# Performance work log

Measured on AMD Instinct MI355X. Metric: run time of the kernel, lower is better.

The kernel has to match this reference:

```python
import jax, jax.numpy as jnp
import numpy as np

H, W = 256, 256          # resolution from __init__ default
FLOW_SCALING = 256.0     # max(resolution)
MAX_TS = 1.0             # events timestamps normalized to [0, 1]
EPS = 1e-9


def _warp_event(events, flow, tref, ts_weights=None):
    """Bilinear splatting of motion-compensated events into per-polarity IWE.
    events: [B,N,4] (ts,x,y,p); flow: [B,N,2]. Returns [B,2,H,W]."""
    ts = events[..., 0]                      # [B,N]
    x = events[..., 1]
    y = events[..., 2]
    pol = events[..., 3]
    # warped (floating-point) positions
    wx = x + (tref - ts) * flow[..., 0] * FLOW_SCALING
    wy = y + (tref - ts) * flow[..., 1] * FLOW_SCALING
    lx = jnp.floor(wx)
    ty = jnp.floor(wy)
    # 4 bilinear corners: [B,4,N]
    cx = jnp.stack([lx, lx + 1.0, lx, lx + 1.0], axis=1)
    cy = jnp.stack([ty, ty, ty + 1.0, ty + 1.0], axis=1)
    w = (jnp.maximum(0.0, 1.0 - jnp.abs(wx[:, None, :] - cx))
         * jnp.maximum(0.0, 1.0 - jnp.abs(wy[:, None, :] - cy)))
    inb = (cx >= 0) & (cx <= W - 1) & (cy >= 0) & (cy <= H - 1)
    w = jnp.where(inb, w, 0.0)
    if ts_weights is not None:               # optional per-event weight (ts)
        w = w * ts_weights[:, None, :]
    flat = (jnp.clip(cy, 0, H - 1) * W + jnp.clip(cx, 0, W - 1)).astype(jnp.int32)

    def splat(f, ww):  # scatter-add one batch element into flat H*W histogram
        return jnp.zeros(H * W, dtype=w.dtype).at[f.reshape(-1)].add(ww.reshape(-1))

    pos_w = jnp.where((pol == 1)[:, None, :], w, 0.0)
    neg_w = jnp.where((pol == -1)[:, None, :], w, 0.0)
    iwe_pos = jax.vmap(splat)(flat, pos_w).reshape(-1, H, W)
    iwe_neg = jax.vmap(splat)(flat, neg_w).reshape(-1, H, W)
    return jnp.stack([iwe_pos, iwe_neg], axis=1)  # [B,2,H,W]


def _warp_contrast(tref, flow, events):
    iwe = _warp_event(events, flow, tref)
    ts_iwe = _warp_event(events, flow, tref, ts_weights=events[..., 0])
    ts_iwe = ts_iwe / (iwe + EPS)
    loss = (ts_iwe ** 2).sum(axis=(1, 2, 3))           # [B]
    non_zero = ((iwe[:, 0] + iwe[:, 1]) > 0).astype(iwe.dtype)
    return loss / non_zero.sum(axis=(1, 2))


def setup_inputs() -> dict:
    key = jax.random.key(0)
    k1, k2, k3, k4, k5 = jax.random.split(key, 5)
    B, N = 2, 1_000_000
    ts = jax.random.uniform(k1, (B, N))
    x = jax.random.uniform(k2, (B, N)) * (W - 1)
    y = jax.random.uniform(k3, (B, N)) * (H - 1)
    p = jnp.where(jax.random.bernoulli(k4, 0.5, (B, N)), 1.0, -1.0)
    events = jnp.stack([ts, x, y, p], axis=-1).astype(jnp.float32)  # [B,N,4]
    flow = (jax.random.normal(k5, (B, N, 2)) * 0.05).astype(jnp.float32)
    return {"events": events, "flow": flow}


def reference(events, flow):
    # temporal contrast-maximization loss: forward + backward warp per pass
    fw = _warp_contrast(MAX_TS, flow, events).sum() / MAX_TS ** 2
    bw = _warp_contrast(0.0, flow, events).sum() / MAX_TS ** 2
    return fw + bw
```

## Files before the change

### kernel.cpp

```cpp
#include <hip/hip_runtime.h>

#define HH 256
#define WW 256
#define HW (HH * WW)
#define BATCH 2
#define NPASS 2
#define EPSF 1e-9f
#define FLOW_SCALE 256.0f

#define NBLK1 1024
#define NCH 2
#define SCAP 1280
#define CAP 2144
#define FPSCALE 16777216.0f
#define FPINV (1.0f / 16777216.0f)


__global__ __launch_bounds__(256) void ew_bin12(
    const float4* __restrict__ events, const float2* __restrict__ flow,
    float* __restrict__ recs, unsigned* __restrict__ tbl, int N) {
  const int b = blockIdx.y;
  const int gblk = b * NBLK1 + blockIdx.x;
  events += (size_t)b * N;
  flow += (size_t)b * N;
  const int EB = (N + NBLK1 - 1) / NBLK1;
  const int i0 = blockIdx.x * EB;
  const int iend = (i0 + EB < N) ? i0 + EB : N;
  const int CEB = (EB + NCH - 1) / NCH;

  __shared__ float stage[SCAP * 3];
  __shared__ unsigned cnt[128], scan[128], start[128], cur[128];
  __shared__ unsigned s_base;
  if (threadIdx.x == 0) s_base = 0u;

  float* __restrict__ myrecs = recs + (size_t)gblk * CAP * 3;

  for (int c = 0; c < NCH; ++c) {
    const int j0 = i0 + c * CEB;
    int j1 = j0 + CEB;
    if (j1 > iend) j1 = iend;
    if (threadIdx.x < 128) {
      cnt[threadIdx.x] = 0u;
      cur[threadIdx.x] = 0u;
    }
    __syncthreads();

    float rwx[2][2], rwy[2][2], rtsp[2];
    unsigned renc[2][2];
    renc[0][0] = renc[0][1] = renc[1][0] = renc[1][1] = 0u;
#pragma unroll
    for (int s = 0; s < 2; ++s) {
      const int i = j0 + s * 256 + (int)threadIdx.x;
      if (i < j1) {
        const float4 e = events[i];
        const float2 f = flow[i];
        rtsp[s] = copysignf(e.x, e.w);
#pragma unroll
        for (int pass = 0; pass < 2; ++pass) {
          const float tref = (pass == 0) ? 1.0f : 0.0f;
          const float dt = tref - e.x;
          const float wx = fmaf(dt * f.x, FLOW_SCALE, e.y);
          const float wy = fmaf(dt * f.y, FLOW_SCALE, e.z);
          rwx[s][pass] = wx;
          rwy[s][pass] = wy;
          const int lx = (int)floorf(wx), ly = (int)floorf(wy);
          int tx = 0, nx = 0, ty = 0, ny = 0;
          if ((unsigned)lx < 256u) {
            tx = lx >> 5;
            nx = ((unsigned)(lx + 1) < 256u && (((lx + 1) >> 5) != tx)) ? 2 : 1;
          } else if ((unsigned)(lx + 1) < 256u) {
            tx = 0;
            nx = 1;
          }
          if ((unsigned)ly < 256u) {
            ty = ly >> 5;
            ny = ((unsigned)(ly + 1) < 256u && (((ly + 1) >> 5) != ty)) ? 2 : 1;
          } else if ((unsigned)(ly + 1) < 256u) {
            ty = 0;
            ny = 1;
          }
          renc[s][pass] = (unsigned)tx | ((unsigned)ty << 3) |
                          ((unsigned)nx << 6) | ((unsigned)ny << 8);
          for (int a = 0; a < ny; ++a)
            for (int c2 = 0; c2 < nx; ++c2)
              atomicAdd(&cnt[pass * 64 + (ty + a) * 8 + tx + c2], 1u);
        }
      }
    }
    __syncthreads();

    if (threadIdx.x < 64) {
      const int l = threadIdx.x;
      unsigned a = cnt[l], bq = cnt[64 + l];
      for (int off = 1; off < 64; off <<= 1) {
        const unsigned ta = __shfl_up(a, off, 64);
        const unsigned tb = __shfl_up(bq, off, 64);
        if (l >= off) {
          a += ta;
          bq += tb;
        }
      }
      const unsigned tot0 = __shfl(a, 63, 64);
      scan[l] = a;
      scan[64 + l] = bq + tot0;
    }
    __syncthreads();

    const unsigned base = s_base;
    unsigned total = scan[127];
    if (total > SCAP) total = SCAP;
    if (total > CAP - base) total = CAP - base;
    if (threadIdx.x < 128) {
      const unsigned c0 = cnt[threadIdx.x];
      const unsigned st = scan[threadIdx.x] - c0;
      unsigned ec = 0u;
      if (st < total) ec = (c0 < total - st) ? c0 : (total - st);
      start[threadIdx.x] = st;
      tbl[((size_t)gblk * 128 + threadIdx.x) * NCH + c] =
          (base + st) | (ec << 16);
    }
    __syncthreads();

#pragma unroll
    for (int s = 0; s < 2; ++s) {
      const int i = j0 + s * 256 + (int)threadIdx.x;
      if (i < j1) {
        const float tsp = rtsp[s];
#pragma unroll
        for (int pass = 0; pass < 2; ++pass) {
          const unsigned enc = renc[s][pass];
          const int nx = (enc >> 6) & 3;
          const int ny = (enc >> 8) & 3;
          if (nx == 0 || ny == 0) continue;
          const int tx = enc & 7;
          const int ty = (enc >> 3) & 7;
          const float wx = rwx[s][pass];
          const float wy = rwy[s][pass];
          for (int a = 0; a < ny; ++a)
            for (int c2 = 0; c2 < nx; ++c2) {
              const int bin = pass * 64 + (ty + a) * 8 + tx + c2;
              const unsigned pos = start[bin] + atomicAdd(&cur[bin], 1u);
              if (pos < total) {
                stage[pos * 3 + 0] = wx;
                stage[pos * 3 + 1] = wy;
                stage[pos * 3 + 2] = tsp;
              }
            }
        }
      }
    }
    __syncthreads();

    const unsigned nf = total * 3;
    float* __restrict__ dst = myrecs + (size_t)base * 3;
    for (unsigned j = threadIdx.x; j < nf; j += 256) dst[j] = stage[j];
    __syncthreads();
    if (threadIdx.x == 0) s_base = base + total;
  }
}

__global__ __launch_bounds__(512) void ew_accum10(
    const float* __restrict__ recs, const uint2* __restrict__ tbl2,
    unsigned long long* __restrict__ histU, int nrep) {
  const int gbin = blockIdx.x;
  const int rep = blockIdx.y;
  const int b = gbin >> 7;
  const int bin127 = gbin & 127;
  const int pass = (gbin >> 6) & 1;
  const int tile = gbin & 63;
  const int tx0 = (tile & 7) * 32;
  const int ty0 = (tile >> 3) * 32;
  const int pb = pass * 2 + b;

  __shared__ unsigned long long lds64[2048];
  for (int j = threadIdx.x; j < 2048; j += 512) lds64[j] = 0ull;
  __syncthreads();

  const int bpr = NBLK1 / nrep;
  const int blk0 = rep * bpr;
  const int grp = threadIdx.x >> 3;
  const int lane = threadIdx.x & 7;
  for (int r = blk0 + grp; r < blk0 + bpr; r += 64) {
    const int gblk = b * NBLK1 + r;
    const float* __restrict__ blkrec = recs + (size_t)gblk * CAP * 3;
    const uint2 tv = tbl2[(size_t)gblk * 128 + bin127];
    const unsigned tvs[2] = {tv.x, tv.y};
#pragma unroll
    for (int c = 0; c < NCH; ++c) {
      const unsigned st = tvs[c] & 0xffffu;
      const unsigned ct = tvs[c] >> 16;
      for (unsigned k = lane; k < ct; k += 8) {
        const float wx = blkrec[(st + k) * 3 + 0];
        const float wy = blkrec[(st + k) * 3 + 1];
        const unsigned tb = __float_as_uint(blkrec[(st + k) * 3 + 2]);
        const int spol = (int)(tb >> 31);
        const float ts = __uint_as_float(tb & 0x7fffffffu);
        const int lx = (int)floorf(wx), ly = (int)floorf(wy);
        const float fx = wx - (float)lx;
        const float fy = wy - (float)ly;
        const float wxs[2] = {1.0f - fx, fx};
        const float wys[2] = {1.0f - fy, fy};
#pragma unroll
        for (int dy = 0; dy < 2; ++dy) {
          const int lcy = ly + dy - ty0;
          if ((unsigned)lcy >= 32u) continue;
#pragma unroll
          for (int dx = 0; dx < 2; ++dx) {
            const int lcx = lx + dx - tx0;
            if ((unsigned)lcx >= 32u) continue;
            const float w = wxs[dx] * wys[dy];
            const unsigned wq = __float2uint_rn(w * FPSCALE);
            const unsigned tq = __float2uint_rn(w * ts * FPSCALE);
            const unsigned long long v =
                ((unsigned long long)wq << 32) | (unsigned long long)tq;
            atomicAdd(&lds64[spol * 1024 + lcy * 32 + lcx], v);
          }
        }
      }
    }
  }
  __syncthreads();

  for (int j = threadIdx.x; j < 2048; j += 512) {
    const int spol = j >> 10;
    const int within = j & 1023;
    const size_t px = (size_t)(ty0 + (within >> 5)) * WW + tx0 + (within & 31);
    histU[(((size_t)rep * 4 + pb) * 2 + spol) * HW + px] = lds64[j];
  }
}

__global__ __launch_bounds__(256) void ew_reduce7(
    const unsigned long long* __restrict__ histU, float* __restrict__ partial,
    int nrep) {
  const int sub = blockIdx.x;
  const int pb = blockIdx.y;
  float loss = 0.0f, nz = 0.0f;
  for (int k = threadIdx.x; k < 1024; k += 256) {
    const int pix = sub * 1024 + k;
    unsigned long long v0 = 0ull, v1 = 0ull;
    for (int r = 0; r < nrep; ++r) {
      v0 += histU[(((size_t)r * 4 + pb) * 2 + 0) * HW + pix];
      v1 += histU[(((size_t)r * 4 + pb) * 2 + 1) * HW + pix];
    }
    const float ip = (float)(unsigned)(v0 >> 32) * FPINV;
    const float tp = (float)(unsigned)(v0 & 0xffffffffull) * FPINV;
    const float in_ = (float)(unsigned)(v1 >> 32) * FPINV;
    const float tn = (float)(unsigned)(v1 & 0xffffffffull) * FPINV;
    const float a = tp / (ip + EPSF);
    const float d = tn / (in_ + EPSF);
    loss += a * a + d * d;
    nz += ((ip + in_) > 0.0f) ? 1.0f : 0.0f;
  }
  for (int off = 32; off > 0; off >>= 1) {
    loss += __shfl_down(loss, off, 64);
    nz += __shfl_down(nz, off, 64);
  }
  __shared__ float sl[4], sn[4];
  const int wid = threadIdx.x >> 6;
  if ((threadIdx.x & 63) == 0) {
    sl[wid] = loss;
    sn[wid] = nz;
  }
  __syncthreads();
  if (threadIdx.x == 0) {
    partial[pb * 64 + sub] = sl[0] + sl[1] + sl[2] + sl[3];
    partial[256 + pb * 64 + sub] = sn[0] + sn[1] + sn[2] + sn[3];
  }
}

__global__ void ew_final3(const float* __restrict__ partial,
                          float* __restrict__ out) {
  if (threadIdx.x == 0 && blockIdx.x == 0) {
    float s = 0.0f;
    for (int pb = 0; pb < 4; ++pb) {
      float L = 0.0f, Z = 0.0f;
      for (int j = 0; j < 64; ++j) {
        L += partial[pb * 64 + j];
        Z += partial[256 + pb * 64 + j];
      }
      s += L / Z;
    }
    out[0] = s;
  }
}

#define HIST_FLOATS (NPASS * BATCH * 4 * HW)

__global__ __launch_bounds__(256) void ew_scatter(
    const float4* __restrict__ events, const float2* __restrict__ flow,
    float* __restrict__ hist, int N) {
  const int b = blockIdx.y;
  events += (size_t)b * N;
  flow += (size_t)b * N;
  float* __restrict__ hb = hist + (size_t)b * 4 * HW;
  for (int i = blockIdx.x * blockDim.x + threadIdx.x; i < N;
       i += gridDim.x * blockDim.x) {
    const float4 e = events[i];
    const float2 f = flow[i];
    const float ts = e.x, x = e.y, y = e.z, p = e.w;
    const int polofs = (p > 0.0f) ? 0 : HW;
#pragma unroll
    for (int pass = 0; pass < NPASS; ++pass) {
      const float tref = (pass == 0) ? 1.0f : 0.0f;
      const float dt = tref - ts;
      const float wx = fmaf(dt * f.x, FLOW_SCALE, x);
      const float wy = fmaf(dt * f.y, FLOW_SCALE, y);
      const float lxf = floorf(wx), tyf = floorf(wy);
      const float fx = wx - lxf, fy = wy - tyf;
      const int lx = (int)lxf, ty = (int)tyf;
      float* __restrict__ wbase = hb + (size_t)pass * BATCH * 4 * HW + polofs;
      float* __restrict__ tbase = wbase + 2 * HW;
      const float w00 = (1.0f - fx) * (1.0f - fy);
      const float w10 = fx * (1.0f - fy);
      const float w01 = (1.0f - fx) * fy;
      const float w11 = fx * fy;
      const int cx0 = lx, cx1 = lx + 1, cy0 = ty, cy1 = ty + 1;
      const bool inx0 = (cx0 >= 0) & (cx0 < WW);
      const bool inx1 = (cx1 >= 0) & (cx1 < WW);
      const bool iny0 = (cy0 >= 0) & (cy0 < HH);
      const bool iny1 = (cy1 >= 0) & (cy1 < HH);
      if (inx0 & iny0) {
        const int pix = cy0 * WW + cx0;
        atomicAdd(wbase + pix, w00);
        atomicAdd(tbase + pix, w00 * ts);
      }
      if (inx1 & iny0) {
        const int pix = cy0 * WW + cx1;
        atomicAdd(wbase + pix, w10);
        atomicAdd(tbase + pix, w10 * ts);
      }
      if (inx0 & iny1) {
        const int pix = cy1 * WW + cx0;
        atomicAdd(wbase + pix, w01);
        atomicAdd(tbase + pix, w01 * ts);
      }
      if (inx1 & iny1) {
        const int pix = cy1 * WW + cx1;
        atomicAdd(wbase + pix, w11);
        atomicAdd(tbase + pix, w11 * ts);
      }
    }
  }
}

__global__ __launch_bounds__(256) void ew_reduce(const float* __restrict__ hist,
                                                 float* __restrict__ partial) {
  const int g = blockIdx.x;
  const float* __restrict__ base = hist + (size_t)g * 4 * HW;
  double loss = 0.0, nz = 0.0;
  for (int pix = threadIdx.x; pix < HW; pix += blockDim.x) {
    const float ip = base[pix];
    const float in_ = base[HW + pix];
    const float tp = base[2 * HW + pix];
    const float tn = base[3 * HW + pix];
    const float a = tp / (ip + EPSF);
    const float c = tn / (in_ + EPSF);
    loss += (double)(a * a) + (double)(c * c);
    if ((ip + in_) > 0.0f) nz += 1.0;
  }
  for (int off = 32; off > 0; off >>= 1) {
    loss += __shfl_down(loss, off, 64);
    nz += __shfl_down(nz, off, 64);
  }
  __shared__ double sl[4], sn[4];
  const int wid = threadIdx.x >> 6;
  if ((threadIdx.x & 63) == 0) {
    sl[wid] = loss;
    sn[wid] = nz;
  }
  __syncthreads();
  if (threadIdx.x == 0) {
    partial[g] = (float)(sl[0] + sl[1] + sl[2] + sl[3]);
    partial[4 + g] = (float)(sn[0] + sn[1] + sn[2] + sn[3]);
  }
}

__global__ void ew_final(const float* __restrict__ partial,
                         float* __restrict__ out) {
  if (threadIdx.x == 0 && blockIdx.x == 0) {
    float s = 0.0f;
    for (int g = 0; g < NPASS * BATCH; ++g) s += partial[g] / partial[4 + g];
    out[0] = s;
  }
}

extern "C" void kernel_launch(void* const* d_in, const int* in_sizes, int n_in,
                              void* d_out, int out_size, void* d_ws,
                              size_t ws_size, hipStream_t stream) {
  const float4* events = (const float4*)d_in[0];
  const float2* flow = (const float2*)d_in[1];
  float* out = (float*)d_out;
  const int N = in_sizes[0] / (4 * BATCH);

  const size_t recs_bytes = (size_t)BATCH * NBLK1 * CAP * 12;
  const size_t tbl_bytes = (size_t)BATCH * NBLK1 * 128 * NCH * sizeof(unsigned);
  const size_t histU1 = (size_t)4 * 2 * HW * sizeof(unsigned long long);
  const size_t tail = 512 * sizeof(float);
  const size_t need1 = recs_bytes + tbl_bytes + histU1 + tail;
  const size_t need2 = recs_bytes + tbl_bytes + 2 * histU1 + tail;
  const size_t need4 = recs_bytes + tbl_bytes + 4 * histU1 + tail;

  if (ws_size >= need1) {
    const int nrep = (ws_size >= need4) ? 4 : ((ws_size >= need2) ? 2 : 1);
    float* recs = (float*)d_ws;
    unsigned* tbl = (unsigned*)((char*)d_ws + recs_bytes);
    unsigned long long* histU = (unsigned long long*)((char*)tbl + tbl_bytes);
    float* partial = (float*)((char*)histU + (size_t)nrep * histU1);

    dim3 bgrid(NBLK1, BATCH);
    ew_bin12<<<bgrid, 256, 0, stream>>>(events, flow, recs, tbl, N);
    dim3 agrid(256, nrep);
    ew_accum10<<<agrid, 512, 0, stream>>>(recs, (const uint2*)tbl, histU, nrep);
    dim3 rgrid(64, 4);
    ew_reduce7<<<rgrid, 256, 0, stream>>>(histU, partial, nrep);
    ew_final3<<<1, 64, 0, stream>>>(partial, out);
  } else {
    float* hist = (float*)d_ws;
    float* partial = hist + HIST_FLOATS;
    hipMemsetAsync(hist, 0, (size_t)HIST_FLOATS * sizeof(float), stream);
    dim3 sgrid(1024, BATCH);
    ew_scatter<<<sgrid, 256, 0, stream>>>(events, flow, hist, N);
    ew_reduce<<<NPASS * BATCH, 256, 0, stream>>>(hist, partial);
    ew_final<<<1, 64, 0, stream>>>(partial, out);
  }
}
```

Baseline: 63.29 us.

## Fuse reduce and final kernels into accumulate via last-block ticket counters

Folds the per-pixel loss reduction and the final scalar combine into the accumulate kernel. A per-tile atomic ticket picks the last replica block, which then sums the replica histograms for its tile and adds fixed-point loss and nonzero counts into global accumulators. A second global ticket lets the last tile write the output. This removes two kernel launches and a pass over the histogram, at the cost of a memset, extra fences and atomics, and fixed-point quantization of the loss sum.

```diff
diff --git a/kernel.cpp b/kernel.cpp
--- a/kernel.cpp
+++ b/kernel.cpp
@@ -159,9 +159,10 @@
   }
 }
 
-__global__ __launch_bounds__(512) void ew_accum10(
+__global__ __launch_bounds__(512) void ew_accum13(
     const float* __restrict__ recs, const uint2* __restrict__ tbl2,
-    unsigned long long* __restrict__ histU, int nrep) {
+    unsigned long long* __restrict__ histU, unsigned* __restrict__ done,
+    unsigned long long* __restrict__ acc, float* __restrict__ out, int nrep) {
   const int gbin = blockIdx.x;
   const int rep = blockIdx.y;
   const int b = gbin >> 7;
@@ -173,6 +174,8 @@
   const int pb = pass * 2 + b;
 
   __shared__ unsigned long long lds64[2048];
+  __shared__ unsigned s_ticket;
+  __shared__ float sl[8], sn[8];
   for (int j = threadIdx.x; j < 2048; j += 512) lds64[j] = 0ull;
   __syncthreads();
 
@@ -227,20 +230,20 @@
     const size_t px = (size_t)(ty0 + (within >> 5)) * WW + tx0 + (within & 31);
     histU[(((size_t)rep * 4 + pb) * 2 + spol) * HW + px] = lds64[j];
   }
-}
-
-__global__ __launch_bounds__(256) void ew_reduce7(
-    const unsigned long long* __restrict__ histU, float* __restrict__ partial,
-    int nrep) {
-  const int sub = blockIdx.x;
-  const int pb = blockIdx.y;
-  float loss = 0.0f, nz = 0.0f;
-  for (int k = threadIdx.x; k < 1024; k += 256) {
-    const int pix = sub * 1024 + k;
+
+  __threadfence();
+  __syncthreads();
+  if (threadIdx.x == 0) s_ticket = atomicAdd(&done[gbin], 1u);
+  __syncthreads();
+  if (s_ticket != (unsigned)(nrep - 1)) return;
+
+  float loss = 0.0f, nzc = 0.0f;
+  for (int p = threadIdx.x; p < 1024; p += 512) {
+    const size_t px = (size_t)(ty0 + (p >> 5)) * WW + tx0 + (p & 31);
     unsigned long long v0 = 0ull, v1 = 0ull;
     for (int r = 0; r < nrep; ++r) {
-      v0 += histU[(((size_t)r * 4 + pb) * 2 + 0) * HW + pix];
-      v1 += histU[(((size_t)r * 4 + pb) * 2 + 1) * HW + pix];
+      v0 += histU[(((size_t)r * 4 + pb) * 2 + 0) * HW + px];
+      v1 += histU[(((size_t)r * 4 + pb) * 2 + 1) * HW + px];
     }
     const float ip = (float)(unsigned)(v0 >> 32) * FPINV;
     const float tp = (float)(unsigned)(v0 & 0xffffffffull) * FPINV;
@@ -249,38 +252,37 @@
     const float a = tp / (ip + EPSF);
     const float d = tn / (in_ + EPSF);
     loss += a * a + d * d;
-    nz += ((ip + in_) > 0.0f) ? 1.0f : 0.0f;
+    nzc += ((ip + in_) > 0.0f) ? 1.0f : 0.0f;
   }
   for (int off = 32; off > 0; off >>= 1) {
     loss += __shfl_down(loss, off, 64);
-    nz += __shfl_down(nz, off, 64);
-  }
-  __shared__ float sl[4], sn[4];
+    nzc += __shfl_down(nzc, off, 64);
+  }
   const int wid = threadIdx.x >> 6;
   if ((threadIdx.x & 63) == 0) {
     sl[wid] = loss;
-    sn[wid] = nz;
+    sn[wid] = nzc;
   }
   __syncthreads();
   if (threadIdx.x == 0) {
-    partial[pb * 64 + sub] = sl[0] + sl[1] + sl[2] + sl[3];
-    partial[256 + pb * 64 + sub] = sn[0] + sn[1] + sn[2] + sn[3];
-  }
-}
-
-__global__ void ew_final3(const float* __restrict__ partial,
-                          float* __restrict__ out) {
-  if (threadIdx.x == 0 && blockIdx.x == 0) {
-    float s = 0.0f;
-    for (int pb = 0; pb < 4; ++pb) {
-      float L = 0.0f, Z = 0.0f;
-      for (int j = 0; j < 64; ++j) {
-        L += partial[pb * 64 + j];
-        Z += partial[256 + pb * 64 + j];
-      }
-      s += L / Z;
-    }
-    out[0] = s;
+    float L = 0.0f, Z = 0.0f;
+    for (int wv = 0; wv < 8; ++wv) {
+      L += sl[wv];
+      Z += sn[wv];
+    }
+    atomicAdd(&acc[pb], (unsigned long long)llrintf(L * FPSCALE));
+    atomicAdd(&acc[4 + pb], (unsigned long long)llrintf(Z));
+    __threadfence();
+    const unsigned t2 = atomicAdd(&done[256], 1u);
+    if (t2 == 255u) {
+      float s = 0.0f;
+      for (int q = 0; q < 4; ++q) {
+        const unsigned long long Lq = atomicAdd(&acc[q], 0ull);
+        const unsigned long long Zq = atomicAdd(&acc[4 + q], 0ull);
+        s += ((float)Lq * FPINV) / (float)Zq;
+      }
+      out[0] = s;
+    }
   }
 }
 
@@ -395,25 +397,26 @@
   const size_t recs_bytes = (size_t)BATCH * NBLK1 * CAP * 12;
   const size_t tbl_bytes = (size_t)BATCH * NBLK1 * 128 * NCH * sizeof(unsigned);
   const size_t histU1 = (size_t)4 * 2 * HW * sizeof(unsigned long long);
-  const size_t tail = 512 * sizeof(float);
-  const size_t need1 = recs_bytes + tbl_bytes + histU1 + tail;
-  const size_t need2 = recs_bytes + tbl_bytes + 2 * histU1 + tail;
-  const size_t need4 = recs_bytes + tbl_bytes + 4 * histU1 + tail;
+  const size_t sync_bytes = 258 * sizeof(unsigned) + 8 * sizeof(unsigned long long);
+  const size_t need1 = recs_bytes + tbl_bytes + histU1 + sync_bytes;
+  const size_t need2 = recs_bytes + tbl_bytes + 2 * histU1 + sync_bytes;
+  const size_t need4 = recs_bytes + tbl_bytes + 4 * histU1 + sync_bytes;
 
   if (ws_size >= need1) {
     const int nrep = (ws_size >= need4) ? 4 : ((ws_size >= need2) ? 2 : 1);
     float* recs = (float*)d_ws;
     unsigned* tbl = (unsigned*)((char*)d_ws + recs_bytes);
     unsigned long long* histU = (unsigned long long*)((char*)tbl + tbl_bytes);
-    float* partial = (float*)((char*)histU + (size_t)nrep * histU1);
-
+    unsigned* done = (unsigned*)((char*)histU + (size_t)nrep * histU1);
+    unsigned long long* acc =
+        (unsigned long long*)((char*)done + 258 * sizeof(unsigned));
+
+    hipMemsetAsync(done, 0, sync_bytes, stream);
     dim3 bgrid(NBLK1, BATCH);
     ew_bin12<<<bgrid, 256, 0, stream>>>(events, flow, recs, tbl, N);
     dim3 agrid(256, nrep);
-    ew_accum10<<<agrid, 512, 0, stream>>>(recs, (const uint2*)tbl, histU, nrep);
-    dim3 rgrid(64, 4);
-    ew_reduce7<<<rgrid, 256, 0, stream>>>(histU, partial, nrep);
-    ew_final3<<<1, 64, 0, stream>>>(partial, out);
+    ew_accum13<<<agrid, 512, 0, stream>>>(recs, (const uint2*)tbl, histU, done,
+                                          acc, out, nrep);
   } else {
     float* hist = (float*)d_ws;
     float* partial = hist + HIST_FLOATS;
```

New measurement: 251.5 us. +297.3%, slower.
